# Kernel optimization log

Hardware: AMD Instinct MI355X
Metric: run time of the kernel (lower is better)

The kernel has to match this reference:

```python
import jax, jax.numpy as jnp
import numpy as np


def _glorot(key, shape):
    lim = np.sqrt(6.0 / (shape[-2] + shape[-1])).astype(np.float32)
    return jax.random.uniform(key, shape, jnp.float32, -lim, lim)


def setup_inputs() -> dict:
    key = jax.random.key(0)
    B, F, K, L = 8192, 256, 32768, 4
    H = 2 * F          # CouplingLayer(feat_size, feat_size * 2) hidden width
    half = F // 2      # affine coupling transforms half the features
    ks = jax.random.split(key, 6)
    return {
        "inputs": jax.random.normal(ks[0], (B, F), jnp.float32),
        "W1": _glorot(ks[1], (L, half, H)),
        "b1": jnp.zeros((L, H), jnp.float32),
        "Ws": _glorot(ks[2], (L, H, half)),
        "bs": jnp.zeros((L, half), jnp.float32),
        "Wt": _glorot(ks[3], (L, H, half)),
        "bt": jnp.zeros((L, half), jnp.float32),
        "prior": _glorot(ks[4], (K, F)),  # VQ codebook, GlorotUniform init as in source
    }


def _forward_flow(x, W1, b1, Ws, bs, Wt, bt):
    """Stack of affine coupling layers; returns (y, log|det J|) per sample."""
    L = W1.shape[0]
    jac = jnp.zeros((x.shape[0],), x.dtype)
    for l in range(L):  # small fixed layer count
        xa, xb = jnp.split(x, 2, axis=1)                 # [B, F/2] each
        h = jax.nn.relu(xa @ W1[l] + b1[l])              # [B, 2F]
        s_raw = h @ Ws[l] + bs[l]                        # [B, F/2]
        s = s_raw if l == L - 1 else jnp.tanh(s_raw)     # last layer: tf.identity
        t = h @ Wt[l] + bt[l]
        yb = xb * jnp.exp(s) + t
        jac = jac + jnp.sum(s, axis=1)
        x = jnp.concatenate([yb, xa], axis=1)            # swap halves for mixing
    return x, jac


def reference(inputs, W1, b1, Ws, bs, Wt, bt, prior):
    sg = jax.lax.stop_gradient
    x, jac = _forward_flow(inputs, W1, b1, Ws, bs, Wt, bt)   # [B, F], [B]
    # pairwise squared distance to codebook: [B, K]
    na = jnp.sum(x * x, axis=1, keepdims=True)               # [B, 1]
    nb = jnp.sum(prior * prior, axis=1)[None, :]             # [1, K]
    d = jnp.maximum(na - 2.0 * (x @ prior.T) + nb, 0.0)      # [B, K]
    target_ind = jnp.argmin(d, axis=1)                       # [B]
    target = prior[target_ind]                               # gather, [B, F]
    loss_1 = jnp.mean(jnp.sum((x - sg(target)) ** 2, axis=1) / 2)
    loss_2 = jnp.mean(jnp.sum((sg(x) - target) ** 2, axis=1) / 2)
    loss = loss_1 + 0.25 * loss_2 - jnp.mean(jac)
    return x, loss
```

## Files before the change

### kernel.cpp

```cpp
#include <hip/hip_runtime.h>
#include <hip/hip_fp8.h>
#include <stdint.h>

#define NB     8192
#define NF     256
#define NHALF  128
#define NHID   512
#define NLAY   4
#define NK     32768

#define SX     (1.0f / 16.0f)
#define SP     (256.0f)

typedef __attribute__((ext_vector_type(8))) short bf16x8;
typedef __attribute__((ext_vector_type(4))) float f32x4;
typedef __attribute__((ext_vector_type(2))) long i64x2;

static __device__ __forceinline__ unsigned short f2bf(float f) {
  union { float f; unsigned int u; } v; v.f = f;
  return (unsigned short)((v.u + 0x7FFFu + ((v.u >> 16) & 1u)) >> 16);
}
static __device__ __forceinline__ float bf2f(unsigned short u) {
  union { unsigned int u; float f; } v; v.u = ((unsigned int)u) << 16; return v.f;
}
static __device__ __forceinline__ unsigned char f2fp8(float f) {
  __hip_fp8_e4m3 q(f);
  return (unsigned char)q.__x;
}
static __device__ __forceinline__ float fp82f(unsigned char b) {
  __hip_fp8_e4m3 q; q.__x = b; return (float)q;
}
static __device__ __forceinline__ int kperm(int k) {
  return ((k >> 3) & 3) * 64 + ((k >> 5) << 3) + (k & 7);
}

static __device__ __forceinline__ void load_lds16(const void* g, void* l) {
  __builtin_amdgcn_global_load_lds(
      (const __attribute__((address_space(1))) unsigned int*)g,
      (__attribute__((address_space(3))) unsigned int*)l, 16, 0, 0);
}

static __device__ __forceinline__ unsigned long long packsi(float v, int idx) {
  unsigned int b = __float_as_uint(v);
  b = (b & 0x80000000u) ? ~b : (b | 0x80000000u);
  return ((unsigned long long)b << 32) | (unsigned int)(~(unsigned int)idx);
}

static __device__ __forceinline__ float fast_tanh(float x) {
  const float xc = fminf(fmaxf(x, -15.f), 15.f);
  const float e2 = __expf(2.f * xc);
  return 1.f - 2.f / (e2 + 1.f);
}

static __device__ __forceinline__ int swadr(int kseg, int nrows, int row, int kin) {
  return (kseg * nrows + row) * 64 + (((kin >> 3) ^ (row & 7)) * 8) + (kin & 7);
}

__global__ __launch_bounds__(256, 2)
void flow_all(const float* __restrict__ in,
              const unsigned short* __restrict__ W1T,
              const unsigned short* __restrict__ W2I,
              const float* __restrict__ b1A,
              const float* __restrict__ bsA,
              const float* __restrict__ btA,
              float* __restrict__ xout,
              unsigned char* __restrict__ xf8,
              float* __restrict__ jac)
{
  __shared__ __align__(16) unsigned short Xb[2][16 * 128];
  __shared__ __align__(16) unsigned short Hs[16 * 64];
  __shared__ __align__(16) unsigned short Bs[2][8192];
  __shared__ float jlds[3][16];
  const int tid = threadIdx.x;
  const int lane = tid & 63, wave = tid >> 6;
  const int q = lane >> 4, c = lane & 15;
  const int m0 = blockIdx.x * 16;

  {
    const unsigned short* W1l = W1T;
#pragma unroll
    for (int u = 0; u < 4; u++) {
      const int chb = (u * 4 + wave) * 64;
      const int ch = chb + lane;
      const int kseg = ch >> 9, cs = ch & 511;
      const int row = cs >> 3, cc = (cs & 7) ^ (row & 7);
      load_lds16(W1l + (size_t)row * 128 + kseg * 64 + cc * 8, Bs[0] + chb * 8);
    }
  }

#pragma unroll
  for (int v = 0; v < 4; v++) {
    const int t4 = tid + v * 256;
    const int row = t4 >> 6, f4 = t4 & 63;
    const float4 d = *(const float4*)(in + (size_t)(m0 + row) * NF + f4 * 4);
    unsigned short* dst = Xb[f4 >> 5];
    const int feat = (f4 & 31) * 4;
    const float vals[4] = {d.x, d.y, d.z, d.w};
#pragma unroll
    for (int u = 0; u < 4; u++) {
      const int fe = feat + u;
      dst[swadr(fe >> 6, 16, row, fe & 63)] = f2bf(vals[u]);
    }
  }

  float jr[4] = {0.f, 0.f, 0.f, 0.f};
  bf16x8 af1[4];
  const f32x4 z = {0.f, 0.f, 0.f, 0.f};
  f32x4 acc2[4];

  for (int gs = 0; gs < 96; gs++) {
    __syncthreads();

    if (gs + 1 < 96) {
      const int g2 = gs + 1;
      const int l2 = g2 / 24, s2 = g2 % 24, nc2 = s2 / 3, t2 = s2 % 3;
      unsigned short* dst = Bs[g2 & 1];
      if (t2 == 0) {
        const unsigned short* W1l = W1T + (size_t)l2 * (NHID * NHALF) + (size_t)nc2 * 64 * 128;
#pragma unroll
        for (int u = 0; u < 4; u++) {
          const int chb = (u * 4 + wave) * 64;
          const int ch = chb + lane;
          const int kseg = ch >> 9, cs = ch & 511;
          const int row = cs >> 3, cc = (cs & 7) ^ (row & 7);
          load_lds16(W1l + (size_t)row * 128 + kseg * 64 + cc * 8, dst + chb * 8);
        }
      } else {
        const unsigned short* W2l = W2I + (size_t)l2 * (NF * NHID) + nc2 * 64 + (t2 - 1) * 32;
#pragma unroll
        for (int u = 0; u < 4; u++) {
          const int chb = (u * 4 + wave) * 64;
          const int ch = chb + lane;
          const int row = ch >> 2;
          const int cc = (ch & 3) ^ ((row >> 1) & 3);
          load_lds16(W2l + (size_t)row * NHID + cc * 8, dst + chb * 8);
        }
      }
    }

    const int l = gs / 24, s = gs % 24, nc8 = s / 3, typ = s % 3;
    const unsigned short* B = Bs[gs & 1];
    unsigned short* XA = Xb[l & 1];
    unsigned short* XB = Xb[1 - (l & 1)];

    if (typ == 0) {
      if (s == 0) {
#pragma unroll
        for (int kw = 0; kw < 4; kw++) {
          const int kch = kw * 4 + q;
          af1[kw] = *(const bf16x8*)(XA + ((kch >> 3) * 16 + c) * 64 +
                                     (((kch & 7) ^ (c & 7)) * 8));
        }
#pragma unroll
        for (int j = 0; j < 4; j++) acc2[j] = z;
      }
      f32x4 acc1 = z;
      const int rb = wave * 16 + c;
#pragma unroll
      for (int kw = 0; kw < 4; kw++) {
        const int kseg = kw >> 1, g = (kw & 1) * 4 + q;
        const bf16x8 bf = *(const bf16x8*)(B + (kseg * 64 + rb) * 64 + ((g ^ (rb & 7)) * 8));
        acc1 = __builtin_amdgcn_mfma_f32_16x16x32_bf16(af1[kw], bf, acc1, 0, 0, 0);
      }
      const int hc = wave * 16 + c;
      const float bb = b1A[l * NHID + nc8 * 64 + hc];
#pragma unroll
      for (int r = 0; r < 4; r++) {
        float v = acc1[r] + bb;
        v = v > 0.f ? v : 0.f;
        Hs[swadr(0, 16, 4 * q + r, hc)] = f2bf(v);
      }
    } else {
      const int half = typ - 1;
      const bf16x8 afh = *(const bf16x8*)(Hs + c * 64 + (((half * 4 + q) ^ (c & 7)) * 8));
#pragma unroll
      for (int j = 0; j < 4; j++) {
        const int rb = wave * 64 + 16 * j + c;
        const bf16x8 bf = *(const bf16x8*)(B + rb * 32 + ((q ^ ((rb >> 1) & 3)) * 8));
        acc2[j] = __builtin_amdgcn_mfma_f32_16x16x32_bf16(afh, bf, acc2[j], 0, 0, 0);
      }
    }

    if (s == 23) {
      const int parity = c & 1;
      const int lastl = (l == NLAY - 1);
      const float* bsl = bsA + l * NHALF;
      const float* btl = btA + l * NHALF;
#pragma unroll
      for (int j = 0; j < 4; j++) {
        const int col = wave * 64 + 16 * j + c;
#pragma unroll
        for (int r = 0; r < 4; r++) {
          const float val = acc2[j][r];
          const float oth = __shfl_xor(val, 1);
          if (!parity) {
            const int feat = col >> 1;
            float sv = val + bsl[feat];
            if (!lastl) sv = fast_tanh(sv);
            const float t = oth + btl[feat];
            const int row = 4 * q + r;
            const int xaddr = swadr(feat >> 6, 16, row, feat & 63);
            const float xb = bf2f(XB[xaddr]);
            const float yb = xb * __expf(sv) + t;
            jr[r] += sv;
            XB[xaddr] = f2bf(yb);
            if (l >= 2) {
              const int k = lastl ? feat : (NHALF + feat);
              const size_t grow = (size_t)(m0 + row) * NF;
              xout[grow + k] = yb;
              xf8[(size_t)(m0 + row) * 256 + kperm(k)] = f2fp8(yb * SX);
            }
          }
        }
      }
    }
  }

  float v0[4];
#pragma unroll
  for (int r = 0; r < 4; r++) {
    float v = jr[r];
    v += __shfl_xor(v, 1); v += __shfl_xor(v, 2);
    v += __shfl_xor(v, 4); v += __shfl_xor(v, 8);
    if (c == 0) {
      if (wave) jlds[wave - 1][4 * q + r] = v;
      else v0[r] = v;
    }
  }
  __syncthreads();
  if (wave == 0 && c == 0) {
#pragma unroll
    for (int r = 0; r < 4; r++) {
      const int row = 4 * q + r;
      jac[m0 + row] = v0[r] + jlds[0][row] + jlds[1][row] + jlds[2][row];
    }
  }
}

__global__ __launch_bounds__(256, 2)
void vq_argmax(const unsigned char* __restrict__ X8,
               const unsigned char* __restrict__ P8,
               const float* __restrict__ nbh,
               unsigned long long* __restrict__ gbest)
{
  __shared__ __align__(16) unsigned char Bs[64 * 256];
  const int tid = threadIdx.x;
  const int lane = tid & 63, wave = tid >> 6;
  const int y = blockIdx.x & 15;
  const int m0 = (blockIdx.x >> 4) * 256;
  const int q = lane >> 4, c = lane & 15;
  const int mw = m0 + wave * 64;

  long af[4][8];
#pragma unroll
  for (int i = 0; i < 4; i++) {
    const unsigned char* xr = X8 + (size_t)(mw + 16 * i + c) * 256 + q * 64;
#pragma unroll
    for (int kc2 = 0; kc2 < 4; kc2++) {
      const i64x2 v = *(const i64x2*)(xr + kc2 * 16);
      af[i][2 * kc2] = v.x; af[i][2 * kc2 + 1] = v.y;
    }
  }

  float bestv[16];
  int besti[16];
#pragma unroll
  for (int t = 0; t < 16; t++) { bestv[t] = -1e30f; besti[t] = 0; }

  for (int nt = 0; nt < 32; nt++) {
    const int n0 = y * 2048 + nt * 64;
    if (nt) __syncthreads();
#pragma unroll
    for (int u = 0; u < 4; u++) {
      const int chb = (u * 4 + wave) * 64;
      const int ch = chb + lane;
      const int row = ch >> 4, gslot = ch & 15;
      load_lds16(P8 + (size_t)(n0 + row) * 256 + (gslot ^ (row & 15)) * 16,
                 Bs + chb * 16);
    }
    __syncthreads();

    const f32x4 z = {0.f, 0.f, 0.f, 0.f};
    f32x4 acc[4][4];
#pragma unroll
    for (int i = 0; i < 4; i++)
#pragma unroll
      for (int j = 0; j < 4; j++) acc[i][j] = z;

#pragma unroll
    for (int kc2 = 0; kc2 < 4; kc2++) {
      const int g = q * 4 + kc2;
#pragma unroll
      for (int j = 0; j < 4; j++) {
        const int rb = 16 * j + c;
        const i64x2 b2 = *(const i64x2*)(Bs + rb * 256 + ((g ^ (rb & 15)) * 16));
#pragma unroll
        for (int i = 0; i < 4; i++) {
          acc[i][j] = __builtin_amdgcn_mfma_f32_16x16x32_fp8_fp8(af[i][2 * kc2],     b2.x, acc[i][j], 0, 0, 0);
          acc[i][j] = __builtin_amdgcn_mfma_f32_16x16x32_fp8_fp8(af[i][2 * kc2 + 1], b2.y, acc[i][j], 0, 0, 0);
        }
      }
    }

#pragma unroll
    for (int j = 0; j < 4; j++) {
      const int col = n0 + 16 * j + c;
      const float nb = nbh[col];
#pragma unroll
      for (int i = 0; i < 4; i++)
#pragma unroll
        for (int r = 0; r < 4; r++) {
          const float sc = acc[i][j][r] - nb;
          const int t = i * 4 + r;
          if (sc > bestv[t]) { bestv[t] = sc; besti[t] = col; }
        }
    }
  }

#pragma unroll
  for (int t = 0; t < 16; t++) {
    float lv = bestv[t]; int li = besti[t];
#pragma unroll
    for (int mk = 8; mk >= 1; mk >>= 1) {
      const float ov = __shfl_xor(lv, mk);
      const int oi = __shfl_xor(li, mk);
      if (ov > lv || (ov == lv && oi < li)) { lv = ov; li = oi; }
    }
    if (c == 0) {
      const int row = mw + 16 * (t >> 2) + q * 4 + (t & 3);
      atomicMax(&gbest[row], packsi(lv, li));
    }
  }
}

__global__ void prep_all(const float* __restrict__ W1,
                         const float* __restrict__ Ws,
                         const float* __restrict__ Wt,
                         const float* __restrict__ prior,
                         unsigned short* __restrict__ W1T,
                         unsigned short* __restrict__ W2I,
                         unsigned char* __restrict__ p8,
                         float* __restrict__ nbh,
                         unsigned long long* __restrict__ gbest,
                         float* __restrict__ accum)
{
  __shared__ float ts[64 * 65];
  const int bx = blockIdx.x;
  const int tid = threadIdx.x;
  if (bx < 2048) {
    const int k = bx * 16 + (tid >> 4);
    const int l16 = tid & 15;
    float s = 0.f;
#pragma unroll
    for (int v = 0; v < 4; v++) {
      const int off = (v * 16 + l16) * 4;
      const float4 d = *(const float4*)(prior + (size_t)k * NF + off);
      uchar4 o;
      o.x = f2fp8(d.x * SP); o.y = f2fp8(d.y * SP);
      o.z = f2fp8(d.z * SP); o.w = f2fp8(d.w * SP);
      *(uchar4*)(p8 + (size_t)k * 256 + kperm(off)) = o;
      const float q0 = fp82f(o.x), q1 = fp82f(o.y), q2 = fp82f(o.z), q3 = fp82f(o.w);
      s += q0 * q0 + q1 * q1 + q2 * q2 + q3 * q3;
    }
#pragma unroll
    for (int mk = 8; mk >= 1; mk >>= 1) s += __shfl_xor(s, mk);
    if (l16 == 0) nbh[k] = 0.5f * s * (SX / SP);
  } else if (bx < 2112) {
    const int job = bx - 2048;
    const int l = job >> 4, t = job & 15;
    const int k0 = (t >> 3) * 64, n0 = (t & 7) * 64;
    const float* src = W1 + (size_t)l * NHALF * NHID;
#pragma unroll
    for (int v = 0; v < 16; v++) {
      const int e = tid + v * 256;
      const int kk = e >> 6, nn = e & 63;
      ts[kk * 65 + nn] = src[(size_t)(k0 + kk) * NHID + n0 + nn];
    }
    __syncthreads();
    unsigned short* dst = W1T + (size_t)l * NHID * NHALF;
#pragma unroll
    for (int v = 0; v < 16; v++) {
      const int e = tid + v * 256;
      const int nn = e >> 6, kk = e & 63;
      dst[(size_t)(n0 + nn) * NHALF + k0 + kk] = f2bf(ts[kk * 65 + nn]);
    }
  } else if (bx < 2240) {
    const int job = bx - 2112;
    const int l = job >> 5, rem = job & 31;
    const int b = rem >> 4;
    const int k0 = ((rem >> 1) & 7) * 64;
    const int f0 = (rem & 1) * 64;
    const float* src = (b ? Wt : Ws) + (size_t)l * NHID * NHALF;
#pragma unroll
    for (int v = 0; v < 16; v++) {
      const int e = tid + v * 256;
      const int kk = e >> 6, nn = e & 63;
      ts[kk * 65 + nn] = src[(size_t)(k0 + kk) * NHALF + f0 + nn];
    }
    __syncthreads();
#pragma unroll
    for (int v = 0; v < 16; v++) {
      const int e = tid + v * 256;
      const int nn = e >> 6, kk = e & 63;
      W2I[((size_t)l * NF + 2 * (f0 + nn) + b) * NHID + k0 + kk] = f2bf(ts[kk * 65 + nn]);
    }
  } else {
    const int idx = (bx - 2240) * 256 + tid;
    if (idx < NB) gbest[idx] = 0ull;
    if (idx < 2) accum[idx] = 0.f;
  }
}

__global__ void vq_finalize(const float* __restrict__ X,
                            const float* __restrict__ prior,
                            const unsigned long long* __restrict__ gbest,
                            const float* __restrict__ jac,
                            float* __restrict__ accum)
{
  const int wave = threadIdx.x >> 6, lane = threadIdx.x & 63;
  const int gw = blockIdx.x * 4 + wave;
  float accd = 0.f, accj = 0.f;
  for (int r = 0; r < 8; r++) {
    const int row = gw * 8 + r;
    const unsigned int idx = ~(unsigned int)(gbest[row]);
    const float* x = X + (size_t)row * NF;
    const float* p = prior + (size_t)idx * NF;
#pragma unroll
    for (int u = 0; u < 4; u++) {
      const int d = lane + u * 64;
      const float df = x[d] - p[d];
      accd += df * df;
    }
    if (lane == 0) accj += jac[row];
  }
#pragma unroll
  for (int mk = 32; mk >= 1; mk >>= 1) {
    accd += __shfl_xor(accd, mk);
    accj += __shfl_xor(accj, mk);
  }
  __shared__ float sd[4], sj[4];
  if (lane == 0) { sd[wave] = accd; sj[wave] = accj; }
  __syncthreads();
  if (threadIdx.x == 0) {
    atomicAdd(&accum[0], sd[0] + sd[1] + sd[2] + sd[3]);
    atomicAdd(&accum[1], sj[0] + sj[1] + sj[2] + sj[3]);
  }
}

__global__ void finalize_loss(const float* __restrict__ acc, float* __restrict__ loss) {
  if (threadIdx.x == 0 && blockIdx.x == 0)
    loss[0] = 1.25f * (0.5f * acc[0] / (float)NB) - acc[1] / (float)NB;
}

extern "C" void kernel_launch(void* const* d_in, const int* in_sizes, int n_in,
                              void* d_out, int out_size, void* d_ws, size_t ws_size,
                              hipStream_t stream)
{
  (void)in_sizes; (void)n_in; (void)out_size; (void)ws_size;
  const float* inputs = (const float*)d_in[0];
  const float* W1 = (const float*)d_in[1];
  const float* b1 = (const float*)d_in[2];
  const float* Ws = (const float*)d_in[3];
  const float* bs = (const float*)d_in[4];
  const float* Wt = (const float*)d_in[5];
  const float* bt = (const float*)d_in[6];
  const float* prior = (const float*)d_in[7];

  char* p = (char*)d_ws;
  auto alloc = [&](size_t bytes) { char* r = p; p += (bytes + 255) & ~(size_t)255; return r; };
  unsigned short* W1T  = (unsigned short*)alloc((size_t)NLAY * NHID * NHALF * 2);
  unsigned short* W2I  = (unsigned short*)alloc((size_t)NLAY * NF * NHID * 2);
  unsigned char* P8    = (unsigned char*)alloc((size_t)NK * 256);
  float* NBH           = (float*)alloc((size_t)NK * 4);
  unsigned char* XF8   = (unsigned char*)alloc((size_t)NB * 256);
  float* JAC           = (float*)alloc((size_t)NB * 4);
  unsigned long long* GBEST = (unsigned long long*)alloc((size_t)NB * 8);
  float* ACC           = (float*)alloc(256);

  float* xout = (float*)d_out;
  float* loss = xout + (size_t)NB * NF;

  prep_all<<<dim3(2272), 256, 0, stream>>>(
      W1, Ws, Wt, prior, W1T, W2I, P8, NBH, GBEST, ACC);

  flow_all<<<dim3(NB / 16), 256, 0, stream>>>(
      inputs, W1T, W2I, b1, bs, bt, xout, XF8, JAC);

  vq_argmax<<<dim3(32 * 16), 256, 0, stream>>>(XF8, P8, NBH, GBEST);
  vq_finalize<<<dim3(256), 256, 0, stream>>>(xout, prior, GBEST, JAC, ACC);
  finalize_loss<<<1, 1, 0, stream>>>(ACC, loss);
}
```

Before: 291.8 us.

## Run flow kernel with one wave per block reading weights from global, split VQ grid

The flow kernel drops from four waves sharing double-buffered LDS weight tiles to a single wave per 16-row block. That wave loads W1/W2 fragments straight from global memory (served by cache) and keeps all 16 output accumulators in registers, which removes the block barriers and the LDS staging. The VQ argmax grid doubles to 32 codebook splits of 1024 entries each, with an occupancy hint of 4, to fill more CUs. The trade-off is more global/L2 traffic for weights, higher register pressure in the flow kernel, and more partial-argmax atomics.

```diff
diff --git a/kernel.cpp b/kernel.cpp
--- a/kernel.cpp
+++ b/kernel.cpp
@@ -56,7 +56,7 @@
   return (kseg * nrows + row) * 64 + (((kin >> 3) ^ (row & 7)) * 8) + (kin & 7);
 }
 
-__global__ __launch_bounds__(256, 2)
+__global__ __launch_bounds__(64)
 void flow_all(const float* __restrict__ in,
               const unsigned short* __restrict__ W1T,
               const unsigned short* __restrict__ W2I,
@@ -69,28 +69,13 @@
 {
   __shared__ __align__(16) unsigned short Xb[2][16 * 128];
   __shared__ __align__(16) unsigned short Hs[16 * 64];
-  __shared__ __align__(16) unsigned short Bs[2][8192];
-  __shared__ float jlds[3][16];
-  const int tid = threadIdx.x;
-  const int lane = tid & 63, wave = tid >> 6;
+  const int lane = threadIdx.x & 63;
   const int q = lane >> 4, c = lane & 15;
   const int m0 = blockIdx.x * 16;
 
-  {
-    const unsigned short* W1l = W1T;
-#pragma unroll
-    for (int u = 0; u < 4; u++) {
-      const int chb = (u * 4 + wave) * 64;
-      const int ch = chb + lane;
-      const int kseg = ch >> 9, cs = ch & 511;
-      const int row = cs >> 3, cc = (cs & 7) ^ (row & 7);
-      load_lds16(W1l + (size_t)row * 128 + kseg * 64 + cc * 8, Bs[0] + chb * 8);
-    }
-  }
-
-#pragma unroll
-  for (int v = 0; v < 4; v++) {
-    const int t4 = tid + v * 256;
+#pragma unroll
+  for (int v = 0; v < 16; v++) {
+    const int t4 = lane + v * 64;
     const int row = t4 >> 6, f4 = t4 & 63;
     const float4 d = *(const float4*)(in + (size_t)(m0 + row) * NF + f4 * 4);
     unsigned short* dst = Xb[f4 >> 5];
@@ -104,140 +89,105 @@
   }
 
   float jr[4] = {0.f, 0.f, 0.f, 0.f};
-  bf16x8 af1[4];
   const f32x4 z = {0.f, 0.f, 0.f, 0.f};
-  f32x4 acc2[4];
-
-  for (int gs = 0; gs < 96; gs++) {
-    __syncthreads();
-
-    if (gs + 1 < 96) {
-      const int g2 = gs + 1;
-      const int l2 = g2 / 24, s2 = g2 % 24, nc2 = s2 / 3, t2 = s2 % 3;
-      unsigned short* dst = Bs[g2 & 1];
-      if (t2 == 0) {
-        const unsigned short* W1l = W1T + (size_t)l2 * (NHID * NHALF) + (size_t)nc2 * 64 * 128;
-#pragma unroll
-        for (int u = 0; u < 4; u++) {
-          const int chb = (u * 4 + wave) * 64;
-          const int ch = chb + lane;
-          const int kseg = ch >> 9, cs = ch & 511;
-          const int row = cs >> 3, cc = (cs & 7) ^ (row & 7);
-          load_lds16(W1l + (size_t)row * 128 + kseg * 64 + cc * 8, dst + chb * 8);
-        }
-      } else {
-        const unsigned short* W2l = W2I + (size_t)l2 * (NF * NHID) + nc2 * 64 + (t2 - 1) * 32;
-#pragma unroll
-        for (int u = 0; u < 4; u++) {
-          const int chb = (u * 4 + wave) * 64;
-          const int ch = chb + lane;
-          const int row = ch >> 2;
-          const int cc = (ch & 3) ^ ((row >> 1) & 3);
-          load_lds16(W2l + (size_t)row * NHID + cc * 8, dst + chb * 8);
-        }
-      }
-    }
-
-    const int l = gs / 24, s = gs % 24, nc8 = s / 3, typ = s % 3;
-    const unsigned short* B = Bs[gs & 1];
+
+  for (int l = 0; l < NLAY; l++) {
+    const unsigned short* W1l = W1T + (size_t)l * NHID * NHALF;
+    const unsigned short* W2l = W2I + (size_t)l * NF * NHID;
+    const float* bsl = bsA + l * NHALF;
+    const float* btl = btA + l * NHALF;
     unsigned short* XA = Xb[l & 1];
     unsigned short* XB = Xb[1 - (l & 1)];
 
-    if (typ == 0) {
-      if (s == 0) {
+    bf16x8 af1[4];
+#pragma unroll
+    for (int kw = 0; kw < 4; kw++) {
+      const int kch = kw * 4 + q;
+      af1[kw] = *(const bf16x8*)(XA + ((kch >> 3) * 16 + c) * 64 +
+                                 (((kch & 7) ^ (c & 7)) * 8));
+    }
+
+    f32x4 acc2[16];
+#pragma unroll
+    for (int j = 0; j < 16; j++) acc2[j] = z;
+
+    for (int ch8 = 0; ch8 < 8; ch8++) {
+#pragma unroll
+      for (int j = 0; j < 4; j++) {
+        const int col = ch8 * 64 + j * 16 + c;
+        f32x4 a = z;
 #pragma unroll
         for (int kw = 0; kw < 4; kw++) {
-          const int kch = kw * 4 + q;
-          af1[kw] = *(const bf16x8*)(XA + ((kch >> 3) * 16 + c) * 64 +
-                                     (((kch & 7) ^ (c & 7)) * 8));
-        }
-#pragma unroll
-        for (int j = 0; j < 4; j++) acc2[j] = z;
+          const bf16x8 bf = *(const bf16x8*)(W1l + (size_t)col * NHALF + kw * 32 + q * 8);
+          a = __builtin_amdgcn_mfma_f32_16x16x32_bf16(af1[kw], bf, a, 0, 0, 0);
+        }
+        const int hc = j * 16 + c;
+        const float bb = b1A[l * NHID + ch8 * 64 + hc];
+#pragma unroll
+        for (int r = 0; r < 4; r++) {
+          float v = a[r] + bb;
+          v = v > 0.f ? v : 0.f;
+          Hs[swadr(0, 16, 4 * q + r, hc)] = f2bf(v);
+        }
       }
-      f32x4 acc1 = z;
-      const int rb = wave * 16 + c;
-#pragma unroll
-      for (int kw = 0; kw < 4; kw++) {
-        const int kseg = kw >> 1, g = (kw & 1) * 4 + q;
-        const bf16x8 bf = *(const bf16x8*)(B + (kseg * 64 + rb) * 64 + ((g ^ (rb & 7)) * 8));
-        acc1 = __builtin_amdgcn_mfma_f32_16x16x32_bf16(af1[kw], bf, acc1, 0, 0, 0);
+      bf16x8 afh[2];
+#pragma unroll
+      for (int kc = 0; kc < 2; kc++) {
+        const int kch = kc * 4 + q;
+        afh[kc] = *(const bf16x8*)(Hs + c * 64 + ((kch ^ (c & 7)) * 8));
       }
-      const int hc = wave * 16 + c;
-      const float bb = b1A[l * NHID + nc8 * 64 + hc];
+#pragma unroll
+      for (int j2 = 0; j2 < 16; j2++) {
+        const int col = j2 * 16 + c;
+#pragma unroll
+        for (int kc = 0; kc < 2; kc++) {
+          const bf16x8 bf = *(const bf16x8*)(W2l + (size_t)col * NHID + ch8 * 64 + kc * 32 + q * 8);
+          acc2[j2] = __builtin_amdgcn_mfma_f32_16x16x32_bf16(afh[kc], bf, acc2[j2], 0, 0, 0);
+        }
+      }
+    }
+
+    const int parity = c & 1;
+    const int lastl = (l == NLAY - 1);
+#pragma unroll
+    for (int j2 = 0; j2 < 16; j2++) {
+      const int col = j2 * 16 + c;
 #pragma unroll
       for (int r = 0; r < 4; r++) {
-        float v = acc1[r] + bb;
-        v = v > 0.f ? v : 0.f;
-        Hs[swadr(0, 16, 4 * q + r, hc)] = f2bf(v);
+        const float val = acc2[j2][r];
+        const float oth = __shfl_xor(val, 1);
+        if (!parity) {
+          const int feat = col >> 1;
+          float sv = val + bsl[feat];
+          if (!lastl) sv = fast_tanh(sv);
+          const float t = oth + btl[feat];
+          const int row = 4 * q + r;
+          const int xaddr = swadr(feat >> 6, 16, row, feat & 63);
+          const float xb = bf2f(XB[xaddr]);
+          const float yb = xb * __expf(sv) + t;
+          jr[r] += sv;
+          XB[xaddr] = f2bf(yb);
+          if (l >= 2) {
+            const int k = lastl ? feat : (NHALF + feat);
+            const size_t grow = (size_t)(m0 + row) * NF;
+            xout[grow + k] = yb;
+            xf8[(size_t)(m0 + row) * 256 + kperm(k)] = f2fp8(yb * SX);
+          }
+        }
       }
-    } else {
-      const int half = typ - 1;
-      const bf16x8 afh = *(const bf16x8*)(Hs + c * 64 + (((half * 4 + q) ^ (c & 7)) * 8));
-#pragma unroll
-      for (int j = 0; j < 4; j++) {
-        const int rb = wave * 64 + 16 * j + c;
-        const bf16x8 bf = *(const bf16x8*)(B + rb * 32 + ((q ^ ((rb >> 1) & 3)) * 8));
-        acc2[j] = __builtin_amdgcn_mfma_f32_16x16x32_bf16(afh, bf, acc2[j], 0, 0, 0);
-      }
-    }
-
-    if (s == 23) {
-      const int parity = c & 1;
-      const int lastl = (l == NLAY - 1);
-      const float* bsl = bsA + l * NHALF;
-      const float* btl = btA + l * NHALF;
-#pragma unroll
-      for (int j = 0; j < 4; j++) {
-        const int col = wave * 64 + 16 * j + c;
-#pragma unroll
-        for (int r = 0; r < 4; r++) {
-          const float val = acc2[j][r];
-          const float oth = __shfl_xor(val, 1);
-          if (!parity) {
-            const int feat = col >> 1;
-            float sv = val + bsl[feat];
-            if (!lastl) sv = fast_tanh(sv);
-            const float t = oth + btl[feat];
-            const int row = 4 * q + r;
-            const int xaddr = swadr(feat >> 6, 16, row, feat & 63);
-            const float xb = bf2f(XB[xaddr]);
-            const float yb = xb * __expf(sv) + t;
-            jr[r] += sv;
-            XB[xaddr] = f2bf(yb);
-            if (l >= 2) {
-              const int k = lastl ? feat : (NHALF + feat);
-              const size_t grow = (size_t)(m0 + row) * NF;
-              xout[grow + k] = yb;
-              xf8[(size_t)(m0 + row) * 256 + kperm(k)] = f2fp8(yb * SX);
-            }
-          }
-        }
-      }
-    }
-  }
-
-  float v0[4];
+    }
+  }
+
 #pragma unroll
   for (int r = 0; r < 4; r++) {
     float v = jr[r];
     v += __shfl_xor(v, 1); v += __shfl_xor(v, 2);
     v += __shfl_xor(v, 4); v += __shfl_xor(v, 8);
-    if (c == 0) {
-      if (wave) jlds[wave - 1][4 * q + r] = v;
-      else v0[r] = v;
-    }
-  }
-  __syncthreads();
-  if (wave == 0 && c == 0) {
-#pragma unroll
-    for (int r = 0; r < 4; r++) {
-      const int row = 4 * q + r;
-      jac[m0 + row] = v0[r] + jlds[0][row] + jlds[1][row] + jlds[2][row];
-    }
-  }
-}
-
-__global__ __launch_bounds__(256, 2)
+    if (c == 0) jac[m0 + 4 * q + r] = v;
+  }
+}
+
+__global__ __launch_bounds__(256, 4)
 void vq_argmax(const unsigned char* __restrict__ X8,
                const unsigned char* __restrict__ P8,
                const float* __restrict__ nbh,
@@ -246,8 +196,8 @@
   __shared__ __align__(16) unsigned char Bs[64 * 256];
   const int tid = threadIdx.x;
   const int lane = tid & 63, wave = tid >> 6;
-  const int y = blockIdx.x & 15;
-  const int m0 = (blockIdx.x >> 4) * 256;
+  const int y = blockIdx.x & 31;
+  const int m0 = (blockIdx.x >> 5) * 256;
   const int q = lane >> 4, c = lane & 15;
   const int mw = m0 + wave * 64;
 
@@ -267,8 +217,8 @@
 #pragma unroll
   for (int t = 0; t < 16; t++) { bestv[t] = -1e30f; besti[t] = 0; }
 
-  for (int nt = 0; nt < 32; nt++) {
-    const int n0 = y * 2048 + nt * 64;
+  for (int nt = 0; nt < 16; nt++) {
+    const int n0 = y * 1024 + nt * 64;
     if (nt) __syncthreads();
 #pragma unroll
     for (int u = 0; u < 4; u++) {
@@ -483,10 +433,10 @@
   prep_all<<<dim3(2272), 256, 0, stream>>>(
       W1, Ws, Wt, prior, W1T, W2I, P8, NBH, GBEST, ACC);
 
-  flow_all<<<dim3(NB / 16), 256, 0, stream>>>(
+  flow_all<<<dim3(NB / 16), 64, 0, stream>>>(
       inputs, W1T, W2I, b1, bs, bt, xout, XF8, JAC);
 
-  vq_argmax<<<dim3(32 * 16), 256, 0, stream>>>(XF8, P8, NBH, GBEST);
+  vq_argmax<<<dim3(32 * 32), 256, 0, stream>>>(XF8, P8, NBH, GBEST);
   vq_finalize<<<dim3(256), 256, 0, stream>>>(xout, prior, GBEST, JAC, ACC);
   finalize_loss<<<1, 1, 0, stream>>>(ACC, loss);
 }
```

After: 659.4 us. 126% more time.
